# Performance work log

Hardware: AMD Instinct MI355X
Metric: run time of the kernel (lower is better)

## Reference

```python
import jax, jax.numpy as jnp
import numpy as np

N = 8192       # num nodes
D_IN = 256     # raw node feature dim
D = 256        # dim_embeddings
E = 65536      # num edges
P = N * (N - 1) // 2  # num unordered pairs (source < sink)


def setup_inputs() -> dict:
    key = jax.random.key(0)
    k1, k2, k3, k4, k5, k6 = jax.random.split(key, 6)
    nodes = jax.random.normal(k1, (N, D_IN), jnp.float32)
    edges = jax.random.randint(k2, (2, E), 0, N, dtype=jnp.int32)  # [2, E] COO
    # encoder: single linear layer emb = nodes @ W_enc + b_enc
    W_enc = jax.random.normal(k3, (D_IN, D), jnp.float32) * 0.02
    b_enc = jnp.zeros((D,), jnp.float32)
    # cls: Linear(2*D, 2) acting on concat(emb[src], emb[snk])
    W_cls = jax.random.normal(k4, (2 * D, 2), jnp.float32) * 0.02
    b_cls = jax.random.normal(k5, (2,), jnp.float32) * 0.02
    return {"nodes": nodes, "edges": edges, "W_enc": W_enc, "b_enc": b_enc,
            "W_cls": W_cls, "b_cls": b_cls}


def reference(nodes, edges, W_enc, b_enc, W_cls, b_cls):
    # encoder
    emb = nodes @ W_enc + b_enc                      # [N, D]
    # cat(emb[s], emb[t]) @ W_cls == emb[s] @ W_cls[:D] + emb[t] @ W_cls[D:]
    # so precompute the two small projections once, then gather per pair.
    A = emb @ W_cls[:D]                              # [N, 2]
    B = emb @ W_cls[D:]                              # [N, 2]
    src, snk = jnp.triu_indices(N, k=1)              # each [P], source < sink
    y = A[src] + B[snk] + b_cls                      # [P, 2] pair logits
    # edge-membership labels: pair (s,t), s<t -> flat index
    # idx = s*(2N - s - 1)//2 + (t - s - 1)
    u, v = edges[0], edges[1]
    valid = u < v                                    # only s<t pairs are checked
    pair_idx = u * (2 * N - u - 1) // 2 + (v - u - 1)
    pair_idx = jnp.where(valid, pair_idx, 0)
    y_true = jnp.zeros((P,), jnp.int32).at[pair_idx].max(valid.astype(jnp.int32))
    return y, y_true
```

## Files before the change

kernel.cpp:

```cpp
#include <hip/hip_runtime.h>

#define NN 8192
#define PPU 33550336u
static const long long PP = (long long)PPU;

typedef float __attribute__((ext_vector_type(4))) fx4;

#define MSI(j) ((j) + ((j) >> 3))

__global__ __launch_bounds__(256) void ab_zero_kernel(
    const float* __restrict__ nodes,
    const float* __restrict__ W_enc,
    const float* __restrict__ b_enc,
    const float* __restrict__ W_cls,
    const float* __restrict__ b_cls,
    float2* __restrict__ Axy,
    float2* __restrict__ Bzw,
    float*  __restrict__ yt)
{
    const int tid = threadIdx.x;
    const int bid = blockIdx.x;

    if (bid >= 256) {
        fx4* base = (fx4*)yt + (unsigned)(bid - 256) * 1024u + (unsigned)tid;
        fx4 z = {0.f, 0.f, 0.f, 0.f};
        __builtin_nontemporal_store(z, base + 0 * 256);
        __builtin_nontemporal_store(z, base + 1 * 256);
        __builtin_nontemporal_store(z, base + 2 * 256);
        __builtin_nontemporal_store(z, base + 3 * 256);
        return;
    }

    __shared__ float  wc[1024];
    __shared__ float4 msv[288];
    __shared__ float  offs[4];

    for (int i = tid; i < 1024; i += 256) wc[i] = W_cls[i];
    __syncthreads();

    {
        const float4* wr  = (const float4*)(W_enc + tid * 256);
        const float4* wa4 = (const float4*)wc;
        const float4* wb4 = (const float4*)(wc + 512);
        float a0 = 0.f, a1 = 0.f, a2 = 0.f, a3 = 0.f;
        #pragma unroll 8
        for (int i = 0; i < 64; ++i) {
            const float4 v   = wr[i];
            const float4 A01 = wa4[2*i],   A23 = wa4[2*i+1];
            const float4 B01 = wb4[2*i],   B23 = wb4[2*i+1];
            a0 += v.x*A01.x + v.y*A01.z + v.z*A23.x + v.w*A23.z;
            a1 += v.x*A01.y + v.y*A01.w + v.z*A23.y + v.w*A23.w;
            a2 += v.x*B01.x + v.y*B01.z + v.z*B23.x + v.w*B23.z;
            a3 += v.x*B01.y + v.y*B01.w + v.z*B23.y + v.w*B23.w;
        }
        msv[MSI(tid)] = make_float4(a0, a1, a2, a3);
    }
    if (tid < 4) {
        const int c = tid & 1, base = (tid < 2) ? 0 : 256;
        float o = 0.f;
        for (int j = 0; j < 256; ++j) o += b_enc[j] * wc[(base + j) * 2 + c];
        if (tid < 2) o += b_cls[tid];
        offs[tid] = o;
    }
    __syncthreads();

    const int gid  = bid * 256 + tid;
    const int n    = gid >> 3;
    const int part = gid & 7;
    float a0 = 0.f, a1 = 0.f, a2 = 0.f, a3 = 0.f;
    const float4* row = (const float4*)(nodes + (long long)n * 256 + part * 32);
    #pragma unroll
    for (int i = 0; i < 8; ++i) {
        const float4 v = row[i];
        const int j = part * 32 + i * 4;
        const float4 m0 = msv[MSI(j+0)];
        const float4 m1 = msv[MSI(j+1)];
        const float4 m2 = msv[MSI(j+2)];
        const float4 m3 = msv[MSI(j+3)];
        a0 += v.x*m0.x + v.y*m1.x + v.z*m2.x + v.w*m3.x;
        a1 += v.x*m0.y + v.y*m1.y + v.z*m2.y + v.w*m3.y;
        a2 += v.x*m0.z + v.y*m1.z + v.z*m2.z + v.w*m3.z;
        a3 += v.x*m0.w + v.y*m1.w + v.z*m2.w + v.w*m3.w;
    }
    #pragma unroll
    for (int d = 1; d < 8; d <<= 1) {
        a0 += __shfl_xor(a0, d);
        a1 += __shfl_xor(a1, d);
        a2 += __shfl_xor(a2, d);
        a3 += __shfl_xor(a3, d);
    }
    if (part == 0) {
        Axy[n] = make_float2(a0 + offs[0], a1 + offs[1]);
        Bzw[n] = make_float2(a2 + offs[2], a3 + offs[3]);
    }
}

__global__ __launch_bounds__(256) void fill_edge_kernel(
    const float2* __restrict__ Axy,
    const float2* __restrict__ Bzw,
    const int*    __restrict__ edges,
    float* __restrict__ y,
    float* __restrict__ yt,
    int E)
{
    const unsigned g = blockIdx.x * 256u + threadIdx.x;

    if (g < (unsigned)E) {
        const int u = edges[g];
        const int v = edges[E + g];
        if (u < v) {
            const unsigned idx = (((unsigned)u * (16383u - (unsigned)u)) >> 1)
                               + (unsigned)(v - u - 1);
            yt[idx] = 1.0f;
        }
    }

    const unsigned p0 = 2u * g;

    const unsigned M    = 16383u;
    const unsigned disc = M * M - 8u * p0;
    const float sq = sqrtf((float)disc);
    int s = (int)(((float)M - sq) * 0.5f);
    s = s < 0 ? 0 : (s > NN - 2 ? NN - 2 : s);
    unsigned rs = ((unsigned)s * (M - (unsigned)s)) >> 1;
    while (p0 < rs)                           { --s; rs -= (unsigned)(NN - 1 - s); }
    while (p0 >= rs + (unsigned)(NN - 1 - s)) { rs += (unsigned)(NN - 1 - s); ++s; }
    int t = (int)(p0 - rs) + s + 1;

    float2 a  = Axy[s];
    float2 b0 = Bzw[t];
    const float o0 = a.x + b0.x, o1 = a.y + b0.y;
    if (++t == NN) { ++s; t = s + 1; a = Axy[s]; }
    float2 b1 = Bzw[t];
    const float o2 = a.x + b1.x, o3 = a.y + b1.y;

    fx4 v = {o0, o1, o2, o3};
    __builtin_nontemporal_store(v, (fx4*)(y + 4u * g));
}

extern "C" void kernel_launch(void* const* d_in, const int* in_sizes, int n_in,
                              void* d_out, int out_size, void* d_ws, size_t ws_size,
                              hipStream_t stream) {
    const float* nodes = (const float*)d_in[0];
    const int*   edges = (const int*)d_in[1];
    const float* W_enc = (const float*)d_in[2];
    const float* b_enc = (const float*)d_in[3];
    const float* W_cls = (const float*)d_in[4];
    const float* b_cls = (const float*)d_in[5];
    const int E = in_sizes[1] / 2;

    float2* Axy = (float2*)d_ws;
    float2* Bzw = Axy + 8192;

    float* y  = (float*)d_out;
    float* yt = (float*)d_out + 2 * PP;

    ab_zero_kernel<<<256 + 8191, 256, 0, stream>>>(
        nodes, W_enc, b_enc, W_cls, b_cls, Axy, Bzw, yt);

    fill_edge_kernel<<<(int)(PPU / 512u), 256, 0, stream>>>(
        Axy, Bzw, edges, y, yt, E);
}
```

Baseline: 78.94 us.

## Build edge labels in a bitmap then expand while writing logits

Instead of zeroing the whole 134MB label array and then scattering ones into it, edges are atomically ORed into a 4MB bitmap held in workspace. A combined fill kernel then writes both the pair logits and the expanded label floats, each exactly once. This removes a full extra write pass over the label output. The cost is an additional kernel launch, atomics, and a dependence on workspace size, with the old two-kernel path kept as a fallback.

```diff
diff --git a/kernel.cpp b/kernel.cpp
--- a/kernel.cpp
+++ b/kernel.cpp
@@ -3,34 +3,19 @@
 #define NN 8192
 #define PPU 33550336u
 static const long long PP = (long long)PPU;
+#define NBMW 1048448u
+#define NBMF 262112u
 
 typedef float __attribute__((ext_vector_type(4))) fx4;
 
 #define MSI(j) ((j) + ((j) >> 3))
 
-__global__ __launch_bounds__(256) void ab_zero_kernel(
-    const float* __restrict__ nodes,
-    const float* __restrict__ W_enc,
-    const float* __restrict__ b_enc,
-    const float* __restrict__ W_cls,
+__device__ __forceinline__ void ab_body(
+    const float* __restrict__ nodes, const float* __restrict__ W_enc,
+    const float* __restrict__ b_enc, const float* __restrict__ W_cls,
     const float* __restrict__ b_cls,
-    float2* __restrict__ Axy,
-    float2* __restrict__ Bzw,
-    float*  __restrict__ yt)
-{
-    const int tid = threadIdx.x;
-    const int bid = blockIdx.x;
-
-    if (bid >= 256) {
-        fx4* base = (fx4*)yt + (unsigned)(bid - 256) * 1024u + (unsigned)tid;
-        fx4 z = {0.f, 0.f, 0.f, 0.f};
-        __builtin_nontemporal_store(z, base + 0 * 256);
-        __builtin_nontemporal_store(z, base + 1 * 256);
-        __builtin_nontemporal_store(z, base + 2 * 256);
-        __builtin_nontemporal_store(z, base + 3 * 256);
-        return;
-    }
-
+    float2* __restrict__ Axy, float2* __restrict__ Bzw, int bid, int tid)
+{
     __shared__ float  wc[1024];
     __shared__ float4 msv[288];
     __shared__ float  offs[4];
@@ -95,29 +80,12 @@
     }
 }
 
-__global__ __launch_bounds__(256) void fill_edge_kernel(
-    const float2* __restrict__ Axy,
-    const float2* __restrict__ Bzw,
-    const int*    __restrict__ edges,
-    float* __restrict__ y,
-    float* __restrict__ yt,
-    int E)
-{
-    const unsigned g = blockIdx.x * 256u + threadIdx.x;
-
-    if (g < (unsigned)E) {
-        const int u = edges[g];
-        const int v = edges[E + g];
-        if (u < v) {
-            const unsigned idx = (((unsigned)u * (16383u - (unsigned)u)) >> 1)
-                               + (unsigned)(v - u - 1);
-            yt[idx] = 1.0f;
-        }
-    }
-
+__device__ __forceinline__ void y_seg(
+    const float2* __restrict__ Axy, const float2* __restrict__ Bzw,
+    float* __restrict__ y, unsigned g)
+{
     const unsigned p0 = 2u * g;
-
-    const unsigned M    = 16383u;
+    const unsigned M  = 16383u;
     const unsigned disc = M * M - 8u * p0;
     const float sq = sqrtf((float)disc);
     int s = (int)(((float)M - sq) * 0.5f);
@@ -132,10 +100,106 @@
     const float o0 = a.x + b0.x, o1 = a.y + b0.y;
     if (++t == NN) { ++s; t = s + 1; a = Axy[s]; }
     float2 b1 = Bzw[t];
-    const float o2 = a.x + b1.x, o3 = a.y + b1.y;
-
-    fx4 v = {o0, o1, o2, o3};
+    fx4 v = {o0, o1, a.x + b1.x, a.y + b1.y};
     __builtin_nontemporal_store(v, (fx4*)(y + 4u * g));
+}
+
+__global__ __launch_bounds__(256) void ab_bmzero_kernel(
+    const float* __restrict__ nodes, const float* __restrict__ W_enc,
+    const float* __restrict__ b_enc, const float* __restrict__ W_cls,
+    const float* __restrict__ b_cls,
+    float2* __restrict__ Axy, float2* __restrict__ Bzw,
+    unsigned* __restrict__ bm)
+{
+    const int tid = threadIdx.x, bid = blockIdx.x;
+    if (bid >= 256) {
+        const unsigned f = (unsigned)(bid - 256) * 256u + (unsigned)tid;
+        if (f < NBMF) {
+            fx4 z = {0.f, 0.f, 0.f, 0.f};
+            __builtin_nontemporal_store(z, (fx4*)bm + f);
+        }
+        return;
+    }
+    ab_body(nodes, W_enc, b_enc, W_cls, b_cls, Axy, Bzw, bid, tid);
+}
+
+__global__ __launch_bounds__(256) void scatter_kernel(
+    const int* __restrict__ edges, unsigned* __restrict__ bm, int E)
+{
+    const int g = blockIdx.x * 256 + threadIdx.x;
+    if (g >= E) return;
+    const int u = edges[g];
+    const int v = edges[E + g];
+    if (u < v) {
+        const unsigned idx = (((unsigned)u * (16383u - (unsigned)u)) >> 1)
+                           + (unsigned)(v - u - 1);
+        atomicOr(&bm[idx >> 5], 1u << (idx & 31u));
+    }
+}
+
+__global__ __launch_bounds__(256) void fill_kernel(
+    const float2* __restrict__ Axy, const float2* __restrict__ Bzw,
+    const unsigned* __restrict__ bm,
+    float* __restrict__ y, float* __restrict__ yt)
+{
+    const unsigned q = blockIdx.x / 9u, r = blockIdx.x % 9u;
+    const int tid = threadIdx.x;
+
+    if (r == 8u) {
+        const unsigned base = q * 1024u + (unsigned)tid;
+        #pragma unroll
+        for (int k = 0; k < 4; ++k) {
+            const unsigned f = base + (unsigned)k * 256u;
+            const unsigned w = bm[f >> 3];
+            const unsigned nib = (w >> ((f & 7u) * 4u)) & 0xFu;
+            fx4 v = { (nib & 1u) ? 1.f : 0.f,
+                      (nib & 2u) ? 1.f : 0.f,
+                      (nib & 4u) ? 1.f : 0.f,
+                      (nib & 8u) ? 1.f : 0.f };
+            __builtin_nontemporal_store(v, (fx4*)yt + f);
+        }
+    } else {
+        const unsigned yblk = q * 8u + r;
+        y_seg(Axy, Bzw, y, yblk * 256u + (unsigned)tid);
+    }
+}
+
+__global__ __launch_bounds__(256) void ab_zero_kernel(
+    const float* __restrict__ nodes, const float* __restrict__ W_enc,
+    const float* __restrict__ b_enc, const float* __restrict__ W_cls,
+    const float* __restrict__ b_cls,
+    float2* __restrict__ Axy, float2* __restrict__ Bzw,
+    float* __restrict__ yt)
+{
+    const int tid = threadIdx.x, bid = blockIdx.x;
+    if (bid >= 256) {
+        fx4* base = (fx4*)yt + (unsigned)(bid - 256) * 1024u + (unsigned)tid;
+        fx4 z = {0.f, 0.f, 0.f, 0.f};
+        __builtin_nontemporal_store(z, base + 0 * 256);
+        __builtin_nontemporal_store(z, base + 1 * 256);
+        __builtin_nontemporal_store(z, base + 2 * 256);
+        __builtin_nontemporal_store(z, base + 3 * 256);
+        return;
+    }
+    ab_body(nodes, W_enc, b_enc, W_cls, b_cls, Axy, Bzw, bid, tid);
+}
+
+__global__ __launch_bounds__(256) void fill_edge_kernel(
+    const float2* __restrict__ Axy, const float2* __restrict__ Bzw,
+    const int* __restrict__ edges,
+    float* __restrict__ y, float* __restrict__ yt, int E)
+{
+    const unsigned g = blockIdx.x * 256u + threadIdx.x;
+    if (g < (unsigned)E) {
+        const int u = edges[g];
+        const int v = edges[E + g];
+        if (u < v) {
+            const unsigned idx = (((unsigned)u * (16383u - (unsigned)u)) >> 1)
+                               + (unsigned)(v - u - 1);
+            yt[idx] = 1.0f;
+        }
+    }
+    y_seg(Axy, Bzw, y, g);
 }
 
 extern "C" void kernel_launch(void* const* d_in, const int* in_sizes, int n_in,
@@ -149,15 +213,22 @@
     const float* b_cls = (const float*)d_in[5];
     const int E = in_sizes[1] / 2;
 
-    float2* Axy = (float2*)d_ws;
-    float2* Bzw = Axy + 8192;
+    float2*   Axy = (float2*)d_ws;
+    float2*   Bzw = Axy + 8192;
+    unsigned* bm  = (unsigned*)(Bzw + 8192);
 
     float* y  = (float*)d_out;
     float* yt = (float*)d_out + 2 * PP;
 
-    ab_zero_kernel<<<256 + 8191, 256, 0, stream>>>(
-        nodes, W_enc, b_enc, W_cls, b_cls, Axy, Bzw, yt);
-
-    fill_edge_kernel<<<(int)(PPU / 512u), 256, 0, stream>>>(
-        Axy, Bzw, edges, y, yt, E);
-}
+    if (ws_size >= 128u * 1024u + NBMW * 4u) {
+        ab_bmzero_kernel<<<1280, 256, 0, stream>>>(
+            nodes, W_enc, b_enc, W_cls, b_cls, Axy, Bzw, bm);
+        scatter_kernel<<<(E + 255) / 256, 256, 0, stream>>>(edges, bm, E);
+        fill_kernel<<<73719, 256, 0, stream>>>(Axy, Bzw, bm, y, yt);
+    } else {
+        ab_zero_kernel<<<256 + 8191, 256, 0, stream>>>(
+            nodes, W_enc, b_enc, W_cls, b_cls, Axy, Bzw, yt);
+        fill_edge_kernel<<<(int)(PPU / 512u), 256, 0, stream>>>(
+            Axy, Bzw, edges, y, yt, E);
+    }
+}
```

Result: slower. 99.46 us (+26.0%).

## Index pair-fill kernel by row via 2D grid instead of sqrt inversion

Applied to the files above, without the earlier changes.

Replaces the flat pair-index launch, which recovers (s,t) per thread with a sqrt and correction loops, by a 2D grid where blockIdx.y is the source row and blockIdx.x tiles the sink range. Each thread now writes two 8-byte float2 outputs instead of one 16-byte vector, and edge label scattering moves to the first column of blocks in the first 256 rows. This removes the per-thread index decoding but launches many idle blocks, about half of the 16x8191 grid, since later rows are short. It also leaves ragged, partially filled blocks at row ends and uses narrower stores.

```diff
diff --git a/kernel.cpp b/kernel.cpp
--- a/kernel.cpp
+++ b/kernel.cpp
@@ -5,6 +5,7 @@
 static const long long PP = (long long)PPU;
 
 typedef float __attribute__((ext_vector_type(4))) fx4;
+typedef float __attribute__((ext_vector_type(2))) fx2;
 
 #define MSI(j) ((j) + ((j) >> 3))
 
@@ -95,7 +96,7 @@
     }
 }
 
-__global__ __launch_bounds__(256) void fill_edge_kernel(
+__global__ __launch_bounds__(256) void fill_row_kernel(
     const float2* __restrict__ Axy,
     const float2* __restrict__ Bzw,
     const int*    __restrict__ edges,
@@ -103,39 +104,44 @@
     float* __restrict__ yt,
     int E)
 {
-    const unsigned g = blockIdx.x * 256u + threadIdx.x;
+    const unsigned s    = blockIdx.y;
+    const unsigned off0 = blockIdx.x * 512u;
+    const unsigned L    = 8191u - s;
+    if (off0 >= L) return;
 
-    if (g < (unsigned)E) {
-        const int u = edges[g];
-        const int v = edges[E + g];
-        if (u < v) {
-            const unsigned idx = (((unsigned)u * (16383u - (unsigned)u)) >> 1)
-                               + (unsigned)(v - u - 1);
-            yt[idx] = 1.0f;
+    const int tid = threadIdx.x;
+
+    if (blockIdx.x == 0 && s < 256u) {
+        const unsigned ge = s * 256u + (unsigned)tid;
+        if (ge < (unsigned)E) {
+            const int u = edges[ge], v = edges[E + ge];
+            if (u < v) {
+                const unsigned idx = (((unsigned)u * (16383u - (unsigned)u)) >> 1)
+                                   + (unsigned)(v - u - 1);
+                yt[idx] = 1.0f;
+            }
         }
     }
 
-    const unsigned p0 = 2u * g;
+    const unsigned rs = (s * (16383u - s)) >> 1;
+    const float2 a = Axy[s];
+    const unsigned o1 = off0 + (unsigned)tid;
+    const unsigned o2 = o1 + 256u;
+    const bool v1 = o1 < L;
+    const bool v2 = o2 < L;
 
-    const unsigned M    = 16383u;
-    const unsigned disc = M * M - 8u * p0;
-    const float sq = sqrtf((float)disc);
-    int s = (int)(((float)M - sq) * 0.5f);
-    s = s < 0 ? 0 : (s > NN - 2 ? NN - 2 : s);
-    unsigned rs = ((unsigned)s * (M - (unsigned)s)) >> 1;
-    while (p0 < rs)                           { --s; rs -= (unsigned)(NN - 1 - s); }
-    while (p0 >= rs + (unsigned)(NN - 1 - s)) { rs += (unsigned)(NN - 1 - s); ++s; }
-    int t = (int)(p0 - rs) + s + 1;
+    float2 b1, b2;
+    if (v1) b1 = Bzw[s + 1u + o1];
+    if (v2) b2 = Bzw[s + 1u + o2];
 
-    float2 a  = Axy[s];
-    float2 b0 = Bzw[t];
-    const float o0 = a.x + b0.x, o1 = a.y + b0.y;
-    if (++t == NN) { ++s; t = s + 1; a = Axy[s]; }
-    float2 b1 = Bzw[t];
-    const float o2 = a.x + b1.x, o3 = a.y + b1.y;
-
-    fx4 v = {o0, o1, o2, o3};
-    __builtin_nontemporal_store(v, (fx4*)(y + 4u * g));
+    if (v1) {
+        fx2 w = {a.x + b1.x, a.y + b1.y};
+        __builtin_nontemporal_store(w, (fx2*)(y + 2u * (rs + o1)));
+    }
+    if (v2) {
+        fx2 w = {a.x + b2.x, a.y + b2.y};
+        __builtin_nontemporal_store(w, (fx2*)(y + 2u * (rs + o2)));
+    }
 }
 
 extern "C" void kernel_launch(void* const* d_in, const int* in_sizes, int n_in,
@@ -158,6 +164,6 @@
     ab_zero_kernel<<<256 + 8191, 256, 0, stream>>>(
         nodes, W_enc, b_enc, W_cls, b_cls, Axy, Bzw, yt);
 
-    fill_edge_kernel<<<(int)(PPU / 512u), 256, 0, stream>>>(
+    fill_row_kernel<<<dim3(16, 8191), 256, 0, stream>>>(
         Axy, Bzw, edges, y, yt, E);
 }
```

Result: slower. 112.0 us (+41.8%).
